# Performance work log

Measured on AMD Instinct MI355X. Metric: run time of the kernel, lower is better.

Reference implementation:

```python
import jax, jax.numpy as jnp
import numpy as np

B, S, HID = 1, 2048, 2048
H, D = 16, 128          # num heads, head_dim (H*D == HID)
L = 32                  # compression / selection block size
NB = S // L             # number of key blocks
NSEL = 8                # top-n selected blocks per query
WIN = 512               # sliding window size
SCALE = 1.0 / np.sqrt(D)
NEG = -1e9


def rotate_half(x):
    x1, x2 = x[..., : x.shape[-1] // 2], x[..., x.shape[-1] // 2 :]
    return jnp.concatenate([-x2, x1], axis=-1)


def rope_tables(dim, end, theta=10000.0):
    freqs = 1.0 / theta ** (jnp.arange(0, dim, 2, dtype=jnp.float32) / dim)
    ang = jnp.outer(jnp.arange(end, dtype=jnp.float32), freqs)  # [end, dim/2]
    cos = jnp.concatenate([jnp.cos(ang), jnp.cos(ang)], axis=-1)  # [end, dim]
    sin = jnp.concatenate([jnp.sin(ang), jnp.sin(ang)], axis=-1)
    return cos, sin


def setup_inputs() -> dict:
    key = jax.random.key(0)
    ks = jax.random.split(key, 10)
    std = 0.02
    return {
        "hidden_states": jax.random.normal(ks[0], (B, S, HID), jnp.float32),
        "Wq": jax.random.normal(ks[1], (HID, H * D), jnp.float32) * std,
        "bq": jnp.zeros((H * D,), jnp.float32),
        "Wk": jax.random.normal(ks[2], (HID, H * D), jnp.float32) * std,
        "bk": jnp.zeros((H * D,), jnp.float32),
        "Wv": jax.random.normal(ks[3], (HID, H * D), jnp.float32) * std,
        "bv": jnp.zeros((H * D,), jnp.float32),
        "Wg": jax.random.normal(ks[4], (H, D, 3), jnp.float32) * std,
        "bg": jnp.zeros((3,), jnp.float32),
    }


def _nsa_forward(hidden_states, Wq, bq, Wk, bk, Wv, bv, Wg, bg):
    # projections -> [B, H, S, D]
    def proj(W, b):
        return (hidden_states @ W + b).reshape(B, S, H, D).transpose(0, 2, 1, 3)

    q, k, v = proj(Wq, bq), proj(Wk, bk), proj(Wv, bv)

    cos, sin = rope_tables(D, S)  # [S, D]
    cos, sin = cos[None, None], sin[None, None]
    q = q * cos + rotate_half(q) * sin
    k = k * cos + rotate_half(k) * sin

    i = jnp.arange(S)
    t = jnp.arange(S)
    causal = t[None, :] <= i[:, None]  # [S, S]

    # ---- compressed branch: block mean-pooled K/V ----
    k_cmp = k.reshape(B, H, NB, L, D).mean(axis=3)  # [B,H,NB,D]
    v_cmp = v.reshape(B, H, NB, L, D).mean(axis=3)
    # block j visible if it ends at or before query position i
    blk_ok = ((jnp.arange(NB) + 1) * L - 1)[None, :] <= i[:, None]  # [S, NB]
    s_cmp = jnp.einsum("bhid,bhjd->bhij", q, k_cmp) * SCALE  # [B,H,S,NB]
    p_cmp = jax.nn.softmax(jnp.where(blk_ok[None, None], s_cmp, NEG), axis=-1)
    has_blk = blk_ok.any(axis=-1).astype(q.dtype)[None, None, :, None]  # [1,1,S,1]
    out_cmp = jnp.einsum("bhij,bhjd->bhid", p_cmp, v_cmp) * has_blk

    # ---- selection branch: top-n blocks from compressed scores ----
    idx = jax.lax.top_k(p_cmp, NSEL)[1]  # [B,H,S,NSEL]
    block_sel = (idx[..., None] == jnp.arange(NB)).any(axis=-2)  # [B,H,S,NB]
    cur_blk = (i[:, None] // L) == jnp.arange(NB)[None, :]  # always include own block
    block_sel = block_sel | cur_blk[None, None]
    tok_sel = jnp.take(block_sel, t // L, axis=-1)  # [B,H,S,S]
    mask_sel = tok_sel & causal[None, None]

    s = jnp.einsum("bhid,bhjd->bhij", q, k) * SCALE
    p_sel = jax.nn.softmax(jnp.where(mask_sel, s, NEG), axis=-1)
    out_sel = jnp.einsum("bhij,bhjd->bhid", p_sel, v)

    # ---- sliding-window branch ----
    mask_win = causal & ((i[:, None] - t[None, :]) < WIN)
    p_win = jax.nn.softmax(jnp.where(mask_win[None, None], s, NEG), axis=-1)
    out_win = jnp.einsum("bhij,bhjd->bhid", p_win, v)

    # ---- gated combine ----
    g = jax.nn.sigmoid(jnp.einsum("bhsd,hdg->bhsg", q, Wg) + bg)  # [B,H,S,3]
    out = (g[..., 0:1] * out_cmp + g[..., 1:2] * out_sel + g[..., 2:3] * out_win)
    return out.transpose(0, 2, 1, 3).reshape(B, S, H * D)


def reference(hidden_states, Wq, bq, Wk, bk, Wv, bv, Wg, bg):
    return _nsa_forward(hidden_states, Wq, bq, Wk, bk, Wv, bv, Wg, bg)
```

## Files before the change

kernel.cpp:

```cpp
#include <hip/hip_runtime.h>


#define SCALE_F 0.08838834764831845f
#define SCL2E   (0.08838834764831845f * 1.4426950408889634f)

typedef short  bf16x8 __attribute__((ext_vector_type(8)));
typedef short  s16x4  __attribute__((ext_vector_type(4)));
typedef float  f32x4  __attribute__((ext_vector_type(4)));

__device__ __forceinline__ unsigned short f2bfu(float x){
    unsigned u = __builtin_bit_cast(unsigned, x);
    u = (u + 0x7FFFu + ((u >> 16) & 1u)) >> 16;
    return (unsigned short)u;
}
__device__ __forceinline__ float bf2f(unsigned short b){
    unsigned u = ((unsigned)b) << 16;
    return __builtin_bit_cast(float, u);
}
__device__ __forceinline__ f32x4 mfma16(bf16x8 a, bf16x8 b, f32x4 c){
    return __builtin_amdgcn_mfma_f32_16x16x32_bf16(a, b, c, 0, 0, 0);
}

__global__ __launch_bounds__(64) void rope_table_k(float* __restrict__ ct,
                                                   float* __restrict__ st){
    int s = blockIdx.x, j = threadIdx.x;
    float fr  = 1.0f / powf(10000.0f, (float)j * (1.0f / 64.0f));
    float ang = (float)s * fr;
    ct[s * 64 + j] = cosf(ang);
    st[s * 64 + j] = sinf(ang);
}

__global__ __launch_bounds__(256) void prep_split(const float* __restrict__ src,
                                                  unsigned short* __restrict__ hi,
                                                  unsigned short* __restrict__ lo){
    size_t i = ((size_t)blockIdx.x * 256 + threadIdx.x) * 4;
    float4 x = *(const float4*)&src[i];
    unsigned short h0 = f2bfu(x.x), h1 = f2bfu(x.y), h2 = f2bfu(x.z), h3 = f2bfu(x.w);
    s16x4 hv; hv[0] = (short)h0; hv[1] = (short)h1; hv[2] = (short)h2; hv[3] = (short)h3;
    *(s16x4*)&hi[i] = hv;
    s16x4 lv;
    lv[0] = (short)f2bfu(x.x - bf2f(h0)); lv[1] = (short)f2bfu(x.y - bf2f(h1));
    lv[2] = (short)f2bfu(x.z - bf2f(h2)); lv[3] = (short)f2bfu(x.w - bf2f(h3));
    *(s16x4*)&lo[i] = lv;
}

__global__ __launch_bounds__(256) void prep_wT(const float* __restrict__ W,
                                               unsigned short* __restrict__ Th,
                                               unsigned short* __restrict__ Tl){
    __shared__ float T[64][65];
    const int k0 = blockIdx.x * 64, n0 = blockIdx.y * 64;
    const int tid = (int)threadIdx.x;
    #pragma unroll
    for (int it = 0; it < 16; ++it){
        int idx = tid + it * 256;
        int r = idx >> 6, c = idx & 63;
        T[c][r] = W[(size_t)(k0 + r) * 2048 + n0 + c];
    }
    __syncthreads();
    #pragma unroll
    for (int it = 0; it < 16; ++it){
        int idx = tid + it * 256;
        int n = idx >> 6, k = idx & 63;
        float v = T[n][k];
        unsigned short h = f2bfu(v);
        Th[(size_t)(n0 + n) * 2048 + k0 + k] = h;
        if (Tl) Tl[(size_t)(n0 + n) * 2048 + k0 + k] = f2bfu(v - bf2f(h));
    }
}

template <int P>
__global__ __launch_bounds__(256) void gemm_bf(
    const unsigned short* __restrict__ Ah, const unsigned short* __restrict__ Al,
    const unsigned short* __restrict__ Bh, const unsigned short* __restrict__ Bl,
    const float* __restrict__ bias,
    float* __restrict__ outF, unsigned short* __restrict__ outT)
{
    const unsigned short* Ap[2] = {Ah, Al};
    const unsigned short* Bp[2] = {Bh, Bl};

    const int bid = (int)blockIdx.x;
    const int xcd = bid & 7, idx = bid >> 3;
    const int m0  = (((xcd >> 1) << 2) + (idx & 3)) * 128;
    const int h   = ((xcd & 1) << 3) + (idx >> 2);

    const int tid = (int)threadIdx.x;
    const int l   = tid & 63, w = tid >> 6;
    const int wr  = w >> 1,  wc = w & 1;
    const int cc  = l & 15,  g  = l >> 4;

    __shared__ short As[P][128][40];
    __shared__ short Bs[P][128][40];

    f32x4 acc[4][4] = {};
    bf16x8 ra[P][2], rb[P][2];

    auto LOADSTEP = [&](int k0){
        #pragma unroll
        for (int p = 0; p < P; ++p)
            #pragma unroll
            for (int it = 0; it < 2; ++it){
                int c = tid + it * 256;
                int row = c >> 2, col8 = (c & 3) * 8;
                ra[p][it] = *(const bf16x8*)&Ap[p][(size_t)(m0 + row) * 2048 + k0 + col8];
                rb[p][it] = *(const bf16x8*)&Bp[p][(size_t)(h * 128 + row) * 2048 + k0 + col8];
            }
    };
    auto STORESTEP = [&](){
        #pragma unroll
        for (int p = 0; p < P; ++p)
            #pragma unroll
            for (int it = 0; it < 2; ++it){
                int c = tid + it * 256;
                int row = c >> 2, col8 = (c & 3) * 8;
                *(bf16x8*)&As[p][row][col8] = ra[p][it];
                *(bf16x8*)&Bs[p][row][col8] = rb[p][it];
            }
    };

    LOADSTEP(0); STORESTEP(); __syncthreads();
    for (int k0 = 0; k0 < 2048; k0 += 32){
        bool more = (k0 + 32) < 2048;
        if (more) LOADSTEP(k0 + 32);

        bf16x8 ah[4], bh[4];
        #pragma unroll
        for (int mt = 0; mt < 4; ++mt)
            ah[mt] = *(const bf16x8*)&As[0][wr * 64 + mt * 16 + cc][g * 8];
        #pragma unroll
        for (int nt = 0; nt < 4; ++nt)
            bh[nt] = *(const bf16x8*)&Bs[0][wc * 64 + nt * 16 + cc][g * 8];
        if (P == 2){
            bf16x8 al[4], bl[4];
            #pragma unroll
            for (int mt = 0; mt < 4; ++mt)
                al[mt] = *(const bf16x8*)&As[P - 1][wr * 64 + mt * 16 + cc][g * 8];
            #pragma unroll
            for (int nt = 0; nt < 4; ++nt)
                bl[nt] = *(const bf16x8*)&Bs[P - 1][wc * 64 + nt * 16 + cc][g * 8];
            #pragma unroll
            for (int mt = 0; mt < 4; ++mt)
                #pragma unroll
                for (int nt = 0; nt < 4; ++nt){
                    acc[mt][nt] = mfma16(ah[mt], bh[nt], acc[mt][nt]);
                    acc[mt][nt] = mfma16(ah[mt], bl[nt], acc[mt][nt]);
                    acc[mt][nt] = mfma16(al[mt], bh[nt], acc[mt][nt]);
                }
        } else {
            #pragma unroll
            for (int mt = 0; mt < 4; ++mt)
                #pragma unroll
                for (int nt = 0; nt < 4; ++nt)
                    acc[mt][nt] = mfma16(ah[mt], bh[nt], acc[mt][nt]);
        }
        __syncthreads();
        if (more){ STORESTEP(); __syncthreads(); }
    }

    #pragma unroll
    for (int mt = 0; mt < 4; ++mt)
        #pragma unroll
        for (int nt = 0; nt < 4; ++nt)
            #pragma unroll
            for (int j = 0; j < 4; ++j){
                int srow = m0 + wr * 64 + mt * 16 + g * 4 + j;
                int col  = wc * 64 + nt * 16 + cc;
                float v = acc[mt][nt][j] + bias[h * 128 + col];
                if (outF) outF[((size_t)h * 2048 + srow) * 128 + col] = v;
                else      outT[((size_t)h * 128 + col) * 2048 + srow] = f2bfu(v);
            }
}

__global__ __launch_bounds__(256) void rope_apply(
    float* __restrict__ qf, float* __restrict__ kf,
    unsigned short* __restrict__ qbb, unsigned short* __restrict__ kbb,
    const float* __restrict__ ct, const float* __restrict__ st)
{
    int idx = blockIdx.x * 256 + (int)threadIdx.x;
    int j = idx & 63;
    int s = (idx >> 6) & 2047;
    int h = (idx >> 17) & 15;
    int a = idx >> 21;
    size_t off = ((size_t)h * 2048 + s) * 128;
    float* p = (a ? kf : qf) + off;
    unsigned short* pb = (a ? kbb : qbb) + off;
    float c = ct[s * 64 + j], sn = st[s * 64 + j];
    float x1 = p[j], x2 = p[j + 64];
    float y1 = x1 * c - x2 * sn;
    float y2 = x2 * c + x1 * sn;
    p[j]      = y1;  p[j + 64]  = y2;
    pb[j] = f2bfu(y1); pb[j + 64] = f2bfu(y2);
}

__global__ __launch_bounds__(256) void cmp_mean(
    const float* __restrict__ kf, const unsigned short* __restrict__ vtbf,
    float* __restrict__ kcmp, float* __restrict__ vcmp)
{
    int idx = blockIdx.x * 256 + (int)threadIdx.x;
    int d  = idx & 127;
    int nb = (idx >> 7) & 63;
    int h  = idx >> 13;
    const float* kp = &kf[((size_t)h * 2048 + nb * 32) * 128 + d];
    float sk = 0.f;
    #pragma unroll
    for (int t = 0; t < 32; ++t) sk += kp[t * 128];
    const unsigned short* vp = &vtbf[((size_t)h * 128 + d) * 2048 + nb * 32];
    float sv = 0.f;
    #pragma unroll
    for (int t = 0; t < 32; ++t) sv += bf2f(vp[t]);
    kcmp[((size_t)h * 64 + nb) * 128 + d] = sk * 0.03125f;
    vcmp[((size_t)h * 64 + nb) * 128 + d] = sv * 0.03125f;
}

__global__ __launch_bounds__(256) void cmp_attn(
    const float* __restrict__ qf, const float* __restrict__ kcmp,
    const float* __restrict__ vcmp,
    const float* __restrict__ Wg, const float* __restrict__ bg,
    float* __restrict__ out, float* __restrict__ gout,
    unsigned long long* __restrict__ bmask)
{
    const int h = blockIdx.y, qt = blockIdx.x, i0 = qt * 64;
    const int tid = (int)threadIdx.x;
    const int l = tid & 63, w = tid >> 6;
    const int ty = tid >> 4, tx = tid & 15;
    const int cc = l & 15, g = l >> 4;

    __shared__ __align__(16) char smem[65536];
    __shared__ float sgl[4][16][3];
    float4* qs4 = (float4*)smem;
    float4* kc4 = (float4*)(smem + 32768);
    unsigned short* vcT = (unsigned short*)smem;
    float* sc = (float*)(smem + 32768);
    unsigned short* ps = (unsigned short*)(smem + 32768 + 17408);

    #pragma unroll
    for (int it = 0; it < 8; ++it){
        int idx = tid + it * 256;
        int row = idx >> 5, c = idx & 31;
        int cs = c ^ ((row >> 2) & 7);
        qs4[row * 32 + cs] = *(const float4*)&qf[((size_t)h * 2048 + i0 + row) * 128 + c * 4];
        kc4[row * 32 + cs] = *(const float4*)&kcmp[((size_t)h * 64 + row) * 128 + c * 4];
    }
    __syncthreads();

    {
        int gi = l & 3, qq = l >> 2;
        if (gi < 3){
            int q = w * 16 + qq;
            float acc = 0.f;
            #pragma unroll
            for (int c = 0; c < 32; ++c){
                float4 qv = qs4[q * 32 + (c ^ ((q >> 2) & 7))];
                const float* wgp = &Wg[(size_t)h * 384 + (c * 4) * 3 + gi];
                acc += qv.x * wgp[0] + qv.y * wgp[3] + qv.z * wgp[6] + qv.w * wgp[9];
            }
            float gv = 1.f / (1.f + expf(-(acc + bg[gi])));
            sgl[w][qq][gi] = gv;
            gout[((size_t)h * 2048 + i0 + q) * 3 + gi] = gv;
        }
    }

    float acc[4][4] = {};
    #pragma unroll 2
    for (int k0 = 0; k0 < 32; ++k0){
        float4 qv[4], kv[4];
        #pragma unroll
        for (int j = 0; j < 4; ++j) qv[j] = qs4[(4 * ty + j) * 32 + (k0 ^ (ty & 7))];
        #pragma unroll
        for (int c = 0; c < 4; ++c) kv[c] = kc4[(4 * tx + c) * 32 + (k0 ^ (tx & 7))];
        #pragma unroll
        for (int j = 0; j < 4; ++j)
            #pragma unroll
            for (int c = 0; c < 4; ++c)
                acc[j][c] += qv[j].x * kv[c].x + qv[j].y * kv[c].y
                           + qv[j].z * kv[c].z + qv[j].w * kv[c].w;
    }
    __syncthreads();

    #pragma unroll
    for (int j = 0; j < 4; ++j){
        int r = 4 * ty + j, i = i0 + r;
        float4 sv;
        float* svp = (float*)&sv;
        #pragma unroll
        for (int c = 0; c < 4; ++c){
            int b = 4 * tx + c;
            svp[c] = (b * 32 + 31 <= i) ? acc[j][c] * SCALE_F : -1e9f;
        }
        *(float4*)&sc[r * 68 + 4 * tx] = sv;
    }
    #pragma unroll
    for (int it = 0; it < 8; ++it){
        int idx = tid + it * 256;
        int jb = idx >> 5, d4 = (idx & 31) * 4;
        float4 vx = *(const float4*)&vcmp[((size_t)h * 64 + jb) * 128 + d4];
        const float* vp = (const float*)&vx;
        #pragma unroll
        for (int jj = 0; jj < 4; ++jj)
            vcT[(d4 + jj) * 72 + jb] = f2bfu(vp[jj]);
    }
    __syncthreads();

    for (int qq = 0; qq < 16; ++qq){
        const int q = w * 16 + qq;
        float s = sc[q * 68 + l];
        float mx = s;
        #pragma unroll
        for (int off = 1; off < 64; off <<= 1) mx = fmaxf(mx, __shfl_xor(mx, off));
        float p = expf(s - mx);
        float sum = p;
        #pragma unroll
        for (int off = 1; off < 64; off <<= 1) sum += __shfl_xor(sum, off);
        p /= sum;
        ps[q * 72 + l] = f2bfu(p);

        unsigned long long sel = 1ULL << ((i0 + q) >> 5);
        unsigned long long key = (1ULL << 45) |
            ((unsigned long long)__builtin_bit_cast(unsigned, p) << 7) |
            (unsigned long long)(63 - l);
        #pragma unroll
        for (int it = 0; it < 8; ++it){
            unsigned long long k2 = key;
            #pragma unroll
            for (int off = 1; off < 64; off <<= 1){
                unsigned long long o = __shfl_xor(k2, off);
                k2 = (o > k2) ? o : k2;
            }
            int wb = 63 - (int)(k2 & 63ULL);
            sel |= 1ULL << wb;
            if (l == wb) key = 0ULL;
        }
        if (l == 0) bmask[(size_t)h * 2048 + i0 + q] = sel;
    }
    __syncthreads();

    f32x4 oacc[8] = {};
    #pragma unroll
    for (int kk = 0; kk < 2; ++kk){
        bf16x8 pa = *(const bf16x8*)&ps[(w * 16 + cc) * 72 + kk * 32 + g * 8];
        #pragma unroll
        for (int nt2 = 0; nt2 < 8; ++nt2){
            bf16x8 vfr = *(const bf16x8*)&vcT[(nt2 * 16 + cc) * 72 + kk * 32 + g * 8];
            oacc[nt2] = mfma16(pa, vfr, oacc[nt2]);
        }
    }
    #pragma unroll
    for (int j = 0; j < 4; ++j){
        int q = w * 16 + g * 4 + j, iq = i0 + q;
        float g0 = sgl[w][g * 4 + j][0];
        float f = (iq >= 31) ? g0 : 0.f;
        #pragma unroll
        for (int nt2 = 0; nt2 < 8; ++nt2)
            out[(size_t)iq * 2048 + h * 128 + nt2 * 16 + cc] = f * oacc[nt2][j];
    }
}

__global__ __launch_bounds__(256) void attn_ws(
    const unsigned short* __restrict__ qbf,
    const unsigned short* __restrict__ kbf,
    const unsigned short* __restrict__ vtbf,
    const float* __restrict__ gates,
    const unsigned long long* __restrict__ bmask,
    float* __restrict__ out)
{
    const int h  = blockIdx.y;
    const int bx = (int)blockIdx.x;
    const bool SEL = bx < 32;
    const int qt = SEL ? 31 - bx : 63 - bx;
    const int i0 = qt * 64;
    const int tid = (int)threadIdx.x;
    const int l = tid & 63, w = tid >> 6;
    const int cc = l & 15,  g = l >> 4;

    __shared__ short Ks[64][136];
    __shared__ short Vt[128][72];
    __shared__ short Ps[4][16][72];

    unsigned long long um = 0;
    if (SEL){
        um = bmask[(size_t)h * 2048 + i0 + l];
        #pragma unroll
        for (int off = 1; off < 64; off <<= 1) um |= __shfl_xor(um, off);
    }

    unsigned long long bm[4];
    int mrow[4];
    #pragma unroll
    for (int j = 0; j < 4; ++j){
        mrow[j] = i0 + w * 16 + g * 4 + j;
        bm[j] = SEL ? bmask[(size_t)h * 2048 + mrow[j]] : 0ULL;
    }

    bf16x8 qfrag[4];
    {
        const unsigned short* qrow = &qbf[((size_t)h * 2048 + i0 + w * 16 + cc) * 128];
        #pragma unroll
        for (int kk = 0; kk < 4; ++kk)
            qfrag[kk] = *(const bf16x8*)&qrow[kk * 32 + g * 8];
    }

    f32x4 oacc[8] = {};
    float mrun[4], lrun[4];
    #pragma unroll
    for (int j = 0; j < 4; ++j){ mrun[j] = -1e30f; lrun[j] = 0.f; }

    const int chlo = SEL ? 0 : (qt > 8 ? qt - 8 : 0);
    auto needed = [&](int ch)->bool {
        return SEL ? (((um >> (2 * ch)) & 3ULL) != 0ULL) : true;
    };

    bf16x8 rk[4], rv[4];
    auto LOADC = [&](int ch){
        #pragma unroll
        for (int it = 0; it < 4; ++it){
            int c = tid + it * 256;
            rk[it] = *(const bf16x8*)&kbf[((size_t)h * 2048 + ch * 64 + (c >> 4)) * 128 + (c & 15) * 8];
            rv[it] = *(const bf16x8*)&vtbf[((size_t)h * 128 + (c >> 3)) * 2048 + ch * 64 + (c & 7) * 8];
        }
    };
    auto STOREC = [&](){
        #pragma unroll
        for (int it = 0; it < 4; ++it){
            int c = tid + it * 256;
            *(bf16x8*)&Ks[c >> 4][(c & 15) * 8] = rk[it];
            *(bf16x8*)&Vt[c >> 3][(c & 7) * 8] = rv[it];
        }
    };

    int cur = chlo;
    while (cur <= qt && !needed(cur)) ++cur;
    LOADC(cur); STOREC(); __syncthreads();

    while (cur <= qt){
        int nxt = cur + 1;
        while (nxt <= qt && !needed(nxt)) ++nxt;
        const bool more = (nxt <= qt);
        if (more) LOADC(nxt);

        f32x4 sacc[4] = {};
        #pragma unroll
        for (int kk = 0; kk < 4; ++kk)
            #pragma unroll
            for (int nt = 0; nt < 4; ++nt){
                bf16x8 kfr = *(const bf16x8*)&Ks[nt * 16 + cc][kk * 32 + g * 8];
                sacc[nt] = mfma16(qfrag[kk], kfr, sacc[nt]);
            }

        const int tbase = cur * 64;
        #pragma unroll
        for (int j = 0; j < 4; ++j){
            const int iq = mrow[j];
            float sj[4]; bool ok[4];
            float mx = -1e30f;
            #pragma unroll
            for (int nt = 0; nt < 4; ++nt){
                int t = tbase + nt * 16 + cc;
                bool o = (t <= iq) &&
                         (SEL ? (((bm[j] >> (t >> 5)) & 1ULL) != 0ULL)
                              : ((iq - t) < 512));
                float s = sacc[nt][j] * SCL2E;
                sj[nt] = s; ok[nt] = o;
                if (o) mx = fmaxf(mx, s);
            }
            #pragma unroll
            for (int off = 1; off < 16; off <<= 1)
                mx = fmaxf(mx, __shfl_xor(mx, off));
            float mnew = fmaxf(mrun[j], mx);
            float alpha = exp2f(mrun[j] - mnew);
            float psum = 0.f;
            #pragma unroll
            for (int nt = 0; nt < 4; ++nt){
                float p = ok[nt] ? exp2f(sj[nt] - mnew) : 0.f;
                psum += p;
                Ps[w][g * 4 + j][nt * 16 + cc] = (short)f2bfu(p);
            }
            #pragma unroll
            for (int off = 1; off < 16; off <<= 1)
                psum += __shfl_xor(psum, off);
            mrun[j] = mnew;
            lrun[j] = lrun[j] * alpha + psum;
            #pragma unroll
            for (int nt2 = 0; nt2 < 8; ++nt2) oacc[nt2][j] *= alpha;
        }
        __syncthreads();

        #pragma unroll
        for (int kk = 0; kk < 2; ++kk){
            bf16x8 pa = *(const bf16x8*)&Ps[w][cc][kk * 32 + g * 8];
            #pragma unroll
            for (int nt2 = 0; nt2 < 8; ++nt2){
                bf16x8 vfr = *(const bf16x8*)&Vt[nt2 * 16 + cc][kk * 32 + g * 8];
                oacc[nt2] = mfma16(pa, vfr, oacc[nt2]);
            }
        }
        __syncthreads();
        if (more){ STOREC(); __syncthreads(); }
        cur = more ? nxt : qt + 1;
    }

    const int GI = SEL ? 1 : 2;
    #pragma unroll
    for (int j = 0; j < 4; ++j){
        const int iq = mrow[j];
        float gv  = gates[((size_t)h * 2048 + iq) * 3 + GI];
        float inv = gv / lrun[j];
        #pragma unroll
        for (int nt2 = 0; nt2 < 8; ++nt2){
            int d = nt2 * 16 + cc;
            atomicAdd(&out[(size_t)iq * 2048 + h * 128 + d], oacc[nt2][j] * inv);
        }
    }
}

extern "C" void kernel_launch(void* const* d_in, const int* in_sizes, int n_in,
                              void* d_out, int out_size, void* d_ws, size_t ws_size,
                              hipStream_t stream)
{
    const float* X  = (const float*)d_in[0];
    const float* Wq = (const float*)d_in[1];
    const float* bq = (const float*)d_in[2];
    const float* Wk = (const float*)d_in[3];
    const float* bk = (const float*)d_in[4];
    const float* Wv = (const float*)d_in[5];
    const float* bv = (const float*)d_in[6];
    const float* Wg = (const float*)d_in[7];
    const float* bg = (const float*)d_in[8];
    float* out = (float*)d_out;

    const size_t MBs = (size_t)1 << 20;
    char* ws = (char*)d_ws;

    unsigned short* Xh  = (unsigned short*)(ws + 0 * MBs);
    unsigned short* Xl  = (unsigned short*)(ws + 8 * MBs);
    unsigned short* WTh = (unsigned short*)(ws + 16 * MBs);
    unsigned short* WTl = (unsigned short*)(ws + 24 * MBs);
    float* qf  = (float*)(ws + 32 * MBs);
    float* kf  = (float*)(ws + 48 * MBs);
    unsigned short* vtbf = (unsigned short*)(ws + 64 * MBs);
    unsigned short* qbf  = (unsigned short*)(ws + 16 * MBs);
    unsigned short* kbf  = (unsigned short*)(ws + 24 * MBs);
    const size_t SM = 72 * MBs;
    float* cost  = (float*)(ws + SM);
    float* sint  = (float*)(ws + SM + 524288);
    float* kcmp  = (float*)(ws + SM + 1048576);
    float* vcmp  = (float*)(ws + SM + 1572864);
    float* gatesb = (float*)(ws + SM + 2097152);
    unsigned long long* bmaskb = (unsigned long long*)(ws + SM + 2490368);

    rope_table_k<<<2048, 64, 0, stream>>>(cost, sint);
    prep_split<<<4096, 256, 0, stream>>>(X, Xh, Xl);

    prep_wT<<<dim3(32, 32), 256, 0, stream>>>(Wq, WTh, WTl);
    gemm_bf<2><<<256, 256, 0, stream>>>(Xh, Xl, WTh, WTl, bq, qf, nullptr);
    prep_wT<<<dim3(32, 32), 256, 0, stream>>>(Wk, WTh, WTl);
    gemm_bf<2><<<256, 256, 0, stream>>>(Xh, Xl, WTh, WTl, bk, kf, nullptr);
    prep_wT<<<dim3(32, 32), 256, 0, stream>>>(Wv, WTh, nullptr);
    gemm_bf<1><<<256, 256, 0, stream>>>(Xh, nullptr, WTh, nullptr, bv, nullptr, vtbf);

    rope_apply<<<16384, 256, 0, stream>>>(qf, kf, qbf, kbf, cost, sint);
    cmp_mean<<<512, 256, 0, stream>>>(kf, vtbf, kcmp, vcmp);
    cmp_attn<<<dim3(32, 16), 256, 0, stream>>>(qf, kcmp, vcmp, Wg, bg,
                                               out, gatesb, bmaskb);
    attn_ws<<<dim3(64, 16), 256, 0, stream>>>(qbf, kbf, vtbf, gatesb, bmaskb, out);
}
```

Measured before the change: 667.6 us.

## Split attention into flash-decoding segments sharing QK scores across sel/win branches

Merges the selection and sliding-window attention passes into one kernel that computes QK^T once per key chunk and reuses the exponentiated scores for both branches. It drops the online max rescaling in favour of a plain exp2 of the scaled scores. Work per query tile is split into 1 to 4 key-range segments so the grid of 1280 blocks is better balanced. Partial outputs and row sums are combined with atomics into workspace buffers, and a finalize kernel applies the gates and normalisation. The costs are extra memsets, atomic traffic and an additional kernel, plus overflow risk if scores grow large without max subtraction.

Result: faster. 591.7 us (-11.4%).

```diff
diff --git a/kernel.cpp b/kernel.cpp
--- a/kernel.cpp
+++ b/kernel.cpp
@@ -354,18 +354,25 @@
     }
 }
 
-__global__ __launch_bounds__(256) void attn_ws(
+__global__ __launch_bounds__(256) void attn_fd(
     const unsigned short* __restrict__ qbf,
     const unsigned short* __restrict__ kbf,
     const unsigned short* __restrict__ vtbf,
-    const float* __restrict__ gates,
     const unsigned long long* __restrict__ bmask,
-    float* __restrict__ out)
+    float* __restrict__ Osel, float* __restrict__ lsel,
+    float* __restrict__ Owin, float* __restrict__ lwin)
 {
-    const int h  = blockIdx.y;
     const int bx = (int)blockIdx.x;
-    const bool SEL = bx < 32;
-    const int qt = SEL ? 31 - bx : 63 - bx;
+    const int h  = bx & 15;
+    const int rr = 79 - (bx >> 4);
+    const int g4 = (rr >= 48) ? 3 : (rr >= 24) ? 2 : (rr >= 8) ? 1 : 0;
+    const int r  = rr - 4 * g4 * (g4 + 1);
+    const int qt = 8 * g4 + r / (g4 + 1);
+    const int seg = r % (g4 + 1);
+    const int nch = qt + 1, nseg = g4 + 1;
+    const int chlo = seg * nch / nseg;
+    const int chhi = (seg + 1) * nch / nseg;
+
     const int i0 = qt * 64;
     const int tid = (int)threadIdx.x;
     const int l = tid & 63, w = tid >> 6;
@@ -375,19 +382,16 @@
     __shared__ short Vt[128][72];
     __shared__ short Ps[4][16][72];
 
-    unsigned long long um = 0;
-    if (SEL){
-        um = bmask[(size_t)h * 2048 + i0 + l];
-        #pragma unroll
-        for (int off = 1; off < 64; off <<= 1) um |= __shfl_xor(um, off);
-    }
+    unsigned long long um = bmask[(size_t)h * 2048 + i0 + l];
+    #pragma unroll
+    for (int off = 1; off < 64; off <<= 1) um |= __shfl_xor(um, off);
 
     unsigned long long bm[4];
     int mrow[4];
     #pragma unroll
     for (int j = 0; j < 4; ++j){
         mrow[j] = i0 + w * 16 + g * 4 + j;
-        bm[j] = SEL ? bmask[(size_t)h * 2048 + mrow[j]] : 0ULL;
+        bm[j] = bmask[(size_t)h * 2048 + mrow[j]];
     }
 
     bf16x8 qfrag[4];
@@ -398,14 +402,11 @@
             qfrag[kk] = *(const bf16x8*)&qrow[kk * 32 + g * 8];
     }
 
-    f32x4 oacc[8] = {};
-    float mrun[4], lrun[4];
-    #pragma unroll
-    for (int j = 0; j < 4; ++j){ mrun[j] = -1e30f; lrun[j] = 0.f; }
-
-    const int chlo = SEL ? 0 : (qt > 8 ? qt - 8 : 0);
+    f32x4 oaccS[8] = {}, oaccW[8] = {};
+    float lsumS[4] = {}, lsumW[4] = {};
+
     auto needed = [&](int ch)->bool {
-        return SEL ? (((um >> (2 * ch)) & 3ULL) != 0ULL) : true;
+        return (ch >= qt - 8) || (((um >> (2 * ch)) & 3ULL) != 0ULL);
     };
 
     bf16x8 rk[4], rv[4];
@@ -427,88 +428,137 @@
     };
 
     int cur = chlo;
-    while (cur <= qt && !needed(cur)) ++cur;
-    LOADC(cur); STOREC(); __syncthreads();
-
-    while (cur <= qt){
-        int nxt = cur + 1;
-        while (nxt <= qt && !needed(nxt)) ++nxt;
-        const bool more = (nxt <= qt);
-        if (more) LOADC(nxt);
-
-        f32x4 sacc[4] = {};
-        #pragma unroll
-        for (int kk = 0; kk < 4; ++kk)
-            #pragma unroll
-            for (int nt = 0; nt < 4; ++nt){
-                bf16x8 kfr = *(const bf16x8*)&Ks[nt * 16 + cc][kk * 32 + g * 8];
-                sacc[nt] = mfma16(qfrag[kk], kfr, sacc[nt]);
-            }
-
-        const int tbase = cur * 64;
-        #pragma unroll
-        for (int j = 0; j < 4; ++j){
-            const int iq = mrow[j];
-            float sj[4]; bool ok[4];
-            float mx = -1e30f;
-            #pragma unroll
-            for (int nt = 0; nt < 4; ++nt){
-                int t = tbase + nt * 16 + cc;
-                bool o = (t <= iq) &&
-                         (SEL ? (((bm[j] >> (t >> 5)) & 1ULL) != 0ULL)
-                              : ((iq - t) < 512));
-                float s = sacc[nt][j] * SCL2E;
-                sj[nt] = s; ok[nt] = o;
-                if (o) mx = fmaxf(mx, s);
-            }
-            #pragma unroll
-            for (int off = 1; off < 16; off <<= 1)
-                mx = fmaxf(mx, __shfl_xor(mx, off));
-            float mnew = fmaxf(mrun[j], mx);
-            float alpha = exp2f(mrun[j] - mnew);
-            float psum = 0.f;
-            #pragma unroll
-            for (int nt = 0; nt < 4; ++nt){
-                float p = ok[nt] ? exp2f(sj[nt] - mnew) : 0.f;
-                psum += p;
-                Ps[w][g * 4 + j][nt * 16 + cc] = (short)f2bfu(p);
-            }
-            #pragma unroll
-            for (int off = 1; off < 16; off <<= 1)
-                psum += __shfl_xor(psum, off);
-            mrun[j] = mnew;
-            lrun[j] = lrun[j] * alpha + psum;
-            #pragma unroll
-            for (int nt2 = 0; nt2 < 8; ++nt2) oacc[nt2][j] *= alpha;
-        }
-        __syncthreads();
-
-        #pragma unroll
-        for (int kk = 0; kk < 2; ++kk){
-            bf16x8 pa = *(const bf16x8*)&Ps[w][cc][kk * 32 + g * 8];
-            #pragma unroll
-            for (int nt2 = 0; nt2 < 8; ++nt2){
-                bf16x8 vfr = *(const bf16x8*)&Vt[nt2 * 16 + cc][kk * 32 + g * 8];
-                oacc[nt2] = mfma16(pa, vfr, oacc[nt2]);
-            }
-        }
-        __syncthreads();
-        if (more){ STOREC(); __syncthreads(); }
-        cur = more ? nxt : qt + 1;
-    }
-
-    const int GI = SEL ? 1 : 2;
+    while (cur < chhi && !needed(cur)) ++cur;
+    if (cur < chhi){
+        LOADC(cur); STOREC(); __syncthreads();
+
+        while (cur < chhi){
+            int nxt = cur + 1;
+            while (nxt < chhi && !needed(nxt)) ++nxt;
+            const bool more = (nxt < chhi);
+            if (more) LOADC(nxt);
+
+            f32x4 sacc[4] = {};
+            #pragma unroll
+            for (int kk = 0; kk < 4; ++kk)
+                #pragma unroll
+                for (int nt = 0; nt < 4; ++nt){
+                    bf16x8 kfr = *(const bf16x8*)&Ks[nt * 16 + cc][kk * 32 + g * 8];
+                    sacc[nt] = mfma16(qfrag[kk], kfr, sacc[nt]);
+                }
+
+            float pe[4][4];
+            #pragma unroll
+            for (int j = 0; j < 4; ++j)
+                #pragma unroll
+                for (int nt = 0; nt < 4; ++nt)
+                    pe[j][nt] = exp2f(sacc[nt][j] * SCL2E);
+
+            const int tbase = cur * 64;
+
+            #pragma unroll
+            for (int j = 0; j < 4; ++j){
+                const int iq = mrow[j];
+                const int row = g * 4 + j;
+                float pacc = 0.f;
+                #pragma unroll
+                for (int nt = 0; nt < 4; ++nt){
+                    int t = tbase + nt * 16 + cc;
+                    bool o = (t <= iq) && (((bm[j] >> (t >> 5)) & 1ULL) != 0ULL);
+                    float p = o ? pe[j][nt] : 0.f;
+                    pacc += p;
+                    Ps[w][row][nt * 16 + cc] = (short)f2bfu(p);
+                }
+                lsumS[j] += pacc;
+            }
+            #pragma unroll
+            for (int kk = 0; kk < 2; ++kk){
+                bf16x8 pa = *(const bf16x8*)&Ps[w][cc][kk * 32 + g * 8];
+                #pragma unroll
+                for (int nt2 = 0; nt2 < 8; ++nt2){
+                    bf16x8 vfr = *(const bf16x8*)&Vt[nt2 * 16 + cc][kk * 32 + g * 8];
+                    oaccS[nt2] = mfma16(pa, vfr, oaccS[nt2]);
+                }
+            }
+
+            if (cur >= qt - 8){
+                #pragma unroll
+                for (int j = 0; j < 4; ++j){
+                    const int iq = mrow[j];
+                    const int row = g * 4 + j;
+                    float pacc = 0.f;
+                    #pragma unroll
+                    for (int nt = 0; nt < 4; ++nt){
+                        int t = tbase + nt * 16 + cc;
+                        bool o = (t <= iq) && ((iq - t) < 512);
+                        float p = o ? pe[j][nt] : 0.f;
+                        pacc += p;
+                        Ps[w][row][nt * 16 + cc] = (short)f2bfu(p);
+                    }
+                    lsumW[j] += pacc;
+                }
+                #pragma unroll
+                for (int kk = 0; kk < 2; ++kk){
+                    bf16x8 pa = *(const bf16x8*)&Ps[w][cc][kk * 32 + g * 8];
+                    #pragma unroll
+                    for (int nt2 = 0; nt2 < 8; ++nt2){
+                        bf16x8 vfr = *(const bf16x8*)&Vt[nt2 * 16 + cc][kk * 32 + g * 8];
+                        oaccW[nt2] = mfma16(pa, vfr, oaccW[nt2]);
+                    }
+                }
+            }
+
+            __syncthreads();
+            if (more){ STOREC(); __syncthreads(); }
+            cur = more ? nxt : chhi;
+        }
+    }
+
     #pragma unroll
     for (int j = 0; j < 4; ++j){
         const int iq = mrow[j];
-        float gv  = gates[((size_t)h * 2048 + iq) * 3 + GI];
-        float inv = gv / lrun[j];
+        float ls = lsumS[j], lw = lsumW[j];
+        #pragma unroll
+        for (int off = 1; off < 16; off <<= 1){
+            ls += __shfl_xor(ls, off);
+            lw += __shfl_xor(lw, off);
+        }
+        if (cc == 0){
+            atomicAdd(&lsel[(size_t)h * 2048 + iq], ls);
+            atomicAdd(&lwin[(size_t)h * 2048 + iq], lw);
+        }
         #pragma unroll
         for (int nt2 = 0; nt2 < 8; ++nt2){
-            int d = nt2 * 16 + cc;
-            atomicAdd(&out[(size_t)iq * 2048 + h * 128 + d], oacc[nt2][j] * inv);
-        }
-    }
+            size_t po = ((size_t)h * 2048 + iq) * 128 + nt2 * 16 + cc;
+            atomicAdd(&Osel[po], oaccS[nt2][j]);
+            atomicAdd(&Owin[po], oaccW[nt2][j]);
+        }
+    }
+}
+
+__global__ __launch_bounds__(256) void finalize(
+    const float* __restrict__ Osel, const float* __restrict__ lsel,
+    const float* __restrict__ Owin, const float* __restrict__ lwin,
+    const float* __restrict__ gates, float* __restrict__ out)
+{
+    int idx = blockIdx.x * 256 + (int)threadIdx.x;
+    int d4 = (idx & 31) * 4;
+    int s  = (idx >> 5) & 2047;
+    int h  = idx >> 16;
+    size_t hs = (size_t)h * 2048 + s;
+    float g1 = gates[hs * 3 + 1], g2 = gates[hs * 3 + 2];
+    float il = g1 / lsel[hs];
+    float iw = g2 / lwin[hs];
+    size_t po = hs * 128 + d4;
+    float4 a = *(const float4*)&Osel[po];
+    float4 b = *(const float4*)&Owin[po];
+    float* op = &out[(size_t)s * 2048 + h * 128 + d4];
+    float4 o = *(const float4*)op;
+    o.x += a.x * il + b.x * iw;
+    o.y += a.y * il + b.y * iw;
+    o.z += a.z * il + b.z * iw;
+    o.w += a.w * il + b.w * iw;
+    *(float4*)op = o;
 }
 
 extern "C" void kernel_launch(void* const* d_in, const int* in_sizes, int n_in,
@@ -538,6 +588,8 @@
     unsigned short* vtbf = (unsigned short*)(ws + 64 * MBs);
     unsigned short* qbf  = (unsigned short*)(ws + 16 * MBs);
     unsigned short* kbf  = (unsigned short*)(ws + 24 * MBs);
+    float* Osel = (float*)(ws + 0 * MBs);
+    float* Owin = (float*)(ws + 32 * MBs);
     const size_t SM = 72 * MBs;
     float* cost  = (float*)(ws + SM);
     float* sint  = (float*)(ws + SM + 524288);
@@ -545,6 +597,8 @@
     float* vcmp  = (float*)(ws + SM + 1572864);
     float* gatesb = (float*)(ws + SM + 2097152);
     unsigned long long* bmaskb = (unsigned long long*)(ws + SM + 2490368);
+    float* lsel = (float*)(ws + SM + 2752512);
+    float* lwin = (float*)(ws + SM + 2883584);
 
     rope_table_k<<<2048, 64, 0, stream>>>(cost, sint);
     prep_split<<<4096, 256, 0, stream>>>(X, Xh, Xl);
@@ -560,5 +614,12 @@
     cmp_mean<<<512, 256, 0, stream>>>(kf, vtbf, kcmp, vcmp);
     cmp_attn<<<dim3(32, 16), 256, 0, stream>>>(qf, kcmp, vcmp, Wg, bg,
                                                out, gatesb, bmaskb);
-    attn_ws<<<dim3(64, 16), 256, 0, stream>>>(qbf, kbf, vtbf, gatesb, bmaskb, out);
-}
+
+    hipMemsetAsync(Osel, 0, 16 * MBs, stream);
+    hipMemsetAsync(Owin, 0, 16 * MBs, stream);
+    hipMemsetAsync(lsel, 0, 262144, stream);
+
+    attn_fd<<<1280, 256, 0, stream>>>(qbf, kbf, vtbf, bmaskb,
+                                      Osel, lsel, Owin, lwin);
+    finalize<<<4096, 256, 0, stream>>>(Osel, lsel, Owin, lwin, gatesb, out);
+}
```
